# Kernel optimization log

Measured on AMD Instinct MI355X. Metric: run time of the kernel, lower is better.

## Reference

```python
import jax, jax.numpy as jnp
import numpy as np

# sparse_shape = grid_size[::-1] + [1,0,0] for grid_size=[1408,1600,40]
Z, Y, X = 41, 1600, 1408
N = 400000
CIN, COUT = 4, 16
EPS = 1e-3  # BatchNorm1d eps from partial(nn.BatchNorm1d, eps=0.001)


def setup_inputs() -> dict:
    # unique active voxel coordinates (submanifold conv assumes no duplicates)
    rng = np.random.default_rng(0)
    pool = Z * Y * X
    raw = rng.integers(0, pool, size=3 * N, dtype=np.int64)
    lin = np.unique(raw)[:N]
    assert lin.size == N
    z = lin // (Y * X)
    rem = lin % (Y * X)
    y = rem // X
    x = rem % X
    coords = np.stack([np.zeros(N, np.int64), z, y, x], axis=1).astype(np.int32)

    key = jax.random.key(0)
    k1, k2 = jax.random.split(key)
    voxel_features = jax.random.normal(k1, (N, CIN), dtype=jnp.float32)
    # SubMConv3d weight: one [CIN,COUT] matrix per kernel offset (27 = 3^3)
    weight = jax.random.normal(k2, (27, CIN, COUT), dtype=jnp.float32) * 0.1
    gamma = jnp.ones((COUT,), dtype=jnp.float32)
    beta = jnp.zeros((COUT,), dtype=jnp.float32)
    return {
        "voxel_features": voxel_features,
        "voxel_coords": jnp.asarray(coords),
        "weight": weight,
        "gamma": gamma,
        "beta": beta,
    }


_OFFSETS = jnp.asarray(
    np.stack(np.meshgrid([-1, 0, 1], [-1, 0, 1], [-1, 0, 1], indexing="ij"), -1
             ).reshape(27, 3),
    dtype=jnp.int32,
)


def _subm_conv(feats, coords, weight):
    """Submanifold sparse 3D conv: outputs only at active voxel sites.

    Rulebook built via sorted linear keys + searchsorted (gather-GEMM).
    """
    zyx = coords[:, 1:4].astype(jnp.int32)                 # [N,3]
    keys = (zyx[:, 0] * Y + zyx[:, 1]) * X + zyx[:, 2]     # [N] unique linear key
    order = jnp.argsort(keys)
    skeys = keys[order]

    nb = zyx[None, :, :] + _OFFSETS[:, None, :]            # [27,N,3]
    inb = ((nb >= 0).all(-1)
           & (nb[..., 0] < Z) & (nb[..., 1] < Y) & (nb[..., 2] < X))
    nkeys = (nb[..., 0] * Y + nb[..., 1]) * X + nb[..., 2]  # [27,N]
    pos = jnp.clip(jnp.searchsorted(skeys, nkeys), 0, N - 1)
    found = inb & (skeys[pos] == nkeys)                    # neighbor is active
    idx = order[pos]                                       # [27,N] row into feats

    gathered = jnp.where(found[..., None], feats[idx], 0.0)  # [27,N,CIN]
    return jnp.einsum("knc,kco->no", gathered, weight)       # [N,COUT]


def reference(voxel_features, voxel_coords, weight, gamma, beta):
    out = _subm_conv(voxel_features, voxel_coords, weight)
    # BatchNorm1d in training mode: normalize over the N (voxel) axis
    mu = out.mean(0)
    var = out.var(0)
    out = (out - mu) * jax.lax.rsqrt(var + EPS) * gamma + beta
    return jax.nn.relu(out)
```

## Files before the change

### kernel.cpp

```cpp
#include <hip/hip_runtime.h>
#include <stdint.h>

#define ZD 41
#define YD 1600
#define XD 1408
#define YXD (YD * XD)
#define NKEYS (ZD * YD * XD)
#define ENT_WORDS (NKEYS / 32)
#define BN_EPS 1e-3f

typedef unsigned long long u64;


__global__ void __launch_bounds__(256) build_index(
    const int4* __restrict__ coords, u64* __restrict__ entry, int n) {
  int i = blockIdx.x * blockDim.x + threadIdx.x;

  {
    int4 cl = coords[n - 1];
    int glast = (((cl.y * YD + cl.z) * XD + cl.w)) >> 5;
    int stride = gridDim.x * blockDim.x;
    for (int g = glast + 1 + i; g < ENT_WORDS; g += stride)
      entry[g] = (u64)(uint32_t)n;
  }

  if (i >= n) return;
  int4 c = coords[i];
  int key = (c.y * YD + c.z) * XD + c.w;
  int g = key >> 5;

  int pkey = __shfl_up(key, 1);
  if ((threadIdx.x & 63) == 0 && i > 0) {
    int4 cp = coords[i - 1];
    pkey = (cp.y * YD + cp.z) * XD + cp.w;
  }
  int pg = (i > 0) ? (pkey >> 5) : -1;

  if (g != pg) {
    for (int gg = pg + 1; gg < g; ++gg) entry[gg] = (u64)(uint32_t)i;
    uint32_t bits = 1u << (key & 31);
    int j = i + 1;
    while (j < n) {
      int4 cj = coords[j];
      int kj = (cj.y * YD + cj.z) * XD + cj.w;
      if ((kj >> 5) != g) break;
      bits |= 1u << (kj & 31);
      ++j;
    }
    entry[g] = ((u64)bits << 32) | (uint32_t)i;
  }
}

__global__ void __launch_bounds__(256) subm_conv(
    const float4* __restrict__ feats, const int4* __restrict__ coords,
    const float* __restrict__ weight, const u64* __restrict__ entry,
    float* __restrict__ out, float* __restrict__ partial, int n) {
  __shared__ float wl[27 * 64];
  __shared__ float swred[4][32];
  for (int t = threadIdx.x; t < 27 * 64; t += 256) wl[t] = weight[t];
  __syncthreads();

  int B = gridDim.x;
  int q = B >> 3, r = B & 7;
  int xcd = blockIdx.x & 7, off = blockIdx.x >> 3;
  int sb = (xcd < r ? xcd * (q + 1) : r * (q + 1) + (xcd - r) * q) + off;
  int i = sb * 256 + (int)threadIdx.x;

  float acc[16];
#pragma unroll
  for (int o = 0; o < 16; o++) acc[o] = 0.f;

  if (i < n) {
    int4 czyx = coords[i];
    int z = czyx.y, y = czyx.z, x = czyx.w;
    int key = (z * YD + y) * XD + x;

    {
      float4 fs = feats[i];
      const float* wp = &wl[13 * 64];
#pragma unroll
      for (int o = 0; o < 16; o++)
        acc[o] = fs.x * wp[o] + fs.y * wp[o + 16] + fs.z * wp[o + 32] +
                 fs.w * wp[o + 48];
    }

    unsigned mask27 = 0;
#pragma unroll
    for (int dzy = 0; dzy < 9; dzy++) {
      const int dz = dzy / 3 - 1, dy = dzy % 3 - 1;
      bool ok = ((unsigned)(z + dz) < (unsigned)ZD) &&
                ((unsigned)(y + dy) < (unsigned)YD);
      int base = key + dz * YXD + dy * XD - 1;
      int g0 = base >> 5;
      u64 e0 = 0, e1 = 0;
      if (ok) {
        e0 = entry[g0];
        e1 = entry[g0 + 1];
      }
      u64 W = (e0 >> 32) | (e1 & 0xFFFFFFFF00000000ull);
      unsigned m3 = (unsigned)(W >> (base & 31)) & 7u;
      mask27 |= m3 << (dzy * 3);
    }
    mask27 &= ~(1u << 13);
    if (x == 0) mask27 &= ~0x1249249u;
    if (x == XD - 1) mask27 &= ~0x4924924u;

    while (mask27) {
      int b = __ffs(mask27) - 1;
      mask27 &= mask27 - 1;
      int dzy = (b * 11) >> 5;
      int rem = b - dzy * 3;
      int dzq = (dzy * 11) >> 5;
      int dyr = dzy - dzq * 3;
      int s = key + (dzq - 1) * YXD + (dyr - 1) * XD + rem - 1;
      int gs = s >> 5;
      u64 e = entry[gs];
      int j = (int)(e & 0xFFFFFFFFull) +
              __popc((uint32_t)(e >> 32) & ((1u << (s & 31)) - 1u));
      float4 f = feats[j];
      const float* wp = &wl[b * 64];
#pragma unroll
      for (int o = 0; o < 16; o++)
        acc[o] += f.x * wp[o] + f.y * wp[o + 16] + f.z * wp[o + 32] +
                  f.w * wp[o + 48];
    }

    float4* o4 = (float4*)(out + (size_t)i * 16);
    o4[0] = make_float4(acc[0], acc[1], acc[2], acc[3]);
    o4[1] = make_float4(acc[4], acc[5], acc[6], acc[7]);
    o4[2] = make_float4(acc[8], acc[9], acc[10], acc[11]);
    o4[3] = make_float4(acc[12], acc[13], acc[14], acc[15]);
  }

  int lane = threadIdx.x & 63, wv = threadIdx.x >> 6;
#pragma unroll
  for (int o = 0; o < 16; o++) {
    float s = acc[o], qq = acc[o] * acc[o];
#pragma unroll
    for (int offx = 32; offx; offx >>= 1) {
      s += __shfl_xor(s, offx);
      qq += __shfl_xor(qq, offx);
    }
    if (lane == 0) {
      swred[wv][o] = s;
      swred[wv][16 + o] = qq;
    }
  }
  __syncthreads();
  if (threadIdx.x < 32) {
    float v = swred[0][threadIdx.x] + swred[1][threadIdx.x] +
              swred[2][threadIdx.x] + swred[3][threadIdx.x];
    partial[(size_t)blockIdx.x * 32 + threadIdx.x] = v;
  }
}

__global__ void __launch_bounds__(1024) bn_finalize(
    const float4* __restrict__ partial4, float* __restrict__ accum, int nb) {
  __shared__ float4 s4[1024];
  int t = threadIdx.x;
  int q = t & 7;
  int row0 = t >> 3;
  float4 v = make_float4(0.f, 0.f, 0.f, 0.f);
  for (int b = row0; b < nb; b += 128) {
    float4 p = partial4[(size_t)b * 8 + q];
    v.x += p.x;
    v.y += p.y;
    v.z += p.z;
    v.w += p.w;
  }
  s4[t] = v;
  __syncthreads();
  for (int half = 64; half >= 1; half >>= 1) {
    if (row0 < half) {
      float4 o = s4[t + half * 8];
      v.x += o.x;
      v.y += o.y;
      v.z += o.z;
      v.w += o.w;
      s4[t] = v;
    }
    __syncthreads();
  }
  if (t < 8) ((float4*)accum)[t] = s4[t];
}

__global__ void __launch_bounds__(256) bn_apply(
    float* __restrict__ out, const float* __restrict__ accum,
    const float* __restrict__ gamma, const float* __restrict__ beta, int n4,
    float invN) {
  __shared__ float sa[16], sb[16];
  int t = threadIdx.x;
  if (t < 16) {
    float mu = accum[t] * invN;
    float var = accum[16 + t] * invN - mu * mu;
    float inv = rsqrtf(var + BN_EPS);
    float a = gamma[t] * inv;
    sa[t] = a;
    sb[t] = beta[t] - mu * a;
  }
  __syncthreads();
  int i = blockIdx.x * 256 + t;
  if (i >= n4) return;
  float4* p = (float4*)out;
  float4 v = p[i];
  int c0 = (i & 3) * 4;
  v.x = fmaxf(v.x * sa[c0 + 0] + sb[c0 + 0], 0.f);
  v.y = fmaxf(v.y * sa[c0 + 1] + sb[c0 + 1], 0.f);
  v.z = fmaxf(v.z * sa[c0 + 2] + sb[c0 + 2], 0.f);
  v.w = fmaxf(v.w * sa[c0 + 3] + sb[c0 + 3], 0.f);
  p[i] = v;
}

extern "C" void kernel_launch(void* const* d_in, const int* in_sizes, int n_in,
                              void* d_out, int out_size, void* d_ws,
                              size_t ws_size, hipStream_t stream) {
  const float4* feats = (const float4*)d_in[0];
  const int4* coords = (const int4*)d_in[1];
  const float* weight = (const float*)d_in[2];
  const float* gamma = (const float*)d_in[3];
  const float* beta = (const float*)d_in[4];
  int n = in_sizes[0] / 4;

  float* accum = (float*)d_ws;
  u64* entry = (u64*)((char*)d_ws + 256);
  float* partial = (float*)((char*)d_ws + 256 + (size_t)ENT_WORDS * 8 + 16);

  int bb = (n + 255) / 256;
  hipLaunchKernelGGL(build_index, dim3(bb), dim3(256), 0, stream, coords,
                     entry, n);
  hipLaunchKernelGGL(subm_conv, dim3(bb), dim3(256), 0, stream, feats, coords,
                     weight, entry, (float*)d_out, partial, n);
  hipLaunchKernelGGL(bn_finalize, dim3(1), dim3(1024), 0, stream,
                     (const float4*)partial, accum, bb);
  int n4 = n * 4;
  hipLaunchKernelGGL(bn_apply, dim3((n4 + 255) / 256), dim3(256), 0, stream,
                     (float*)d_out, accum, gamma, beta, n4, 1.0f / n);
}
```

Measured before the change: 123.8 us.

## Fuse index build, conv, and batchnorm into one cooperative kernel with grid syncs

Replaces the four-kernel pipeline with one cooperative kernel. It builds the bitmap index, runs the sparse conv, reduces the BN statistics hierarchically and applies BN+ReLU, separated by grid.sync barriers. The conv outputs stay in registers until normalization, so the separate pass that reads and writes the output again is gone, along with the launch gaps. In exchange it needs the whole grid (about 1563 blocks) to be co-resident under launch_bounds(256,7), and it adds three grid-wide barriers. If residency cannot be met it falls back to the old path.

```diff
diff --git a/kernel.cpp b/kernel.cpp
--- a/kernel.cpp
+++ b/kernel.cpp
@@ -1,5 +1,8 @@
 #include <hip/hip_runtime.h>
+#include <hip/hip_cooperative_groups.h>
 #include <stdint.h>
+
+namespace cg = cooperative_groups;
 
 #define ZD 41
 #define YD 1600
@@ -12,59 +15,64 @@
 typedef unsigned long long u64;
 
 
-__global__ void __launch_bounds__(256) build_index(
-    const int4* __restrict__ coords, u64* __restrict__ entry, int n) {
-  int i = blockIdx.x * blockDim.x + threadIdx.x;
-
-  {
-    int4 cl = coords[n - 1];
-    int glast = (((cl.y * YD + cl.z) * XD + cl.w)) >> 5;
-    int stride = gridDim.x * blockDim.x;
-    for (int g = glast + 1 + i; g < ENT_WORDS; g += stride)
-      entry[g] = (u64)(uint32_t)n;
-  }
-
-  if (i >= n) return;
-  int4 c = coords[i];
-  int key = (c.y * YD + c.z) * XD + c.w;
-  int g = key >> 5;
-
-  int pkey = __shfl_up(key, 1);
-  if ((threadIdx.x & 63) == 0 && i > 0) {
-    int4 cp = coords[i - 1];
-    pkey = (cp.y * YD + cp.z) * XD + cp.w;
-  }
-  int pg = (i > 0) ? (pkey >> 5) : -1;
-
-  if (g != pg) {
-    for (int gg = pg + 1; gg < g; ++gg) entry[gg] = (u64)(uint32_t)i;
-    uint32_t bits = 1u << (key & 31);
-    int j = i + 1;
-    while (j < n) {
-      int4 cj = coords[j];
-      int kj = (cj.y * YD + cj.z) * XD + cj.w;
-      if ((kj >> 5) != g) break;
-      bits |= 1u << (kj & 31);
-      ++j;
-    }
-    entry[g] = ((u64)bits << 32) | (uint32_t)i;
-  }
-}
-
-__global__ void __launch_bounds__(256) subm_conv(
+__global__ void __launch_bounds__(256, 7) fused_all(
     const float4* __restrict__ feats, const int4* __restrict__ coords,
-    const float* __restrict__ weight, const u64* __restrict__ entry,
-    float* __restrict__ out, float* __restrict__ partial, int n) {
+    const float* __restrict__ weight, const float* __restrict__ gamma,
+    const float* __restrict__ beta, u64* __restrict__ entry,
+    float* __restrict__ partial, float* __restrict__ partial2,
+    float* __restrict__ out, int n, int nb, float invN) {
+  cg::grid_group grid = cg::this_grid();
+  const int tid = threadIdx.x;
+
   __shared__ float wl[27 * 64];
   __shared__ float swred[4][32];
-  for (int t = threadIdx.x; t < 27 * 64; t += 256) wl[t] = weight[t];
+  __shared__ float red2[8][32];
+  __shared__ float redv[32];
+  __shared__ float sa[16], sbv[16];
+
+  {
+    int ia = blockIdx.x * 256 + tid;
+    int4 cl = coords[n - 1];
+    int glast = ((cl.y * YD + cl.z) * XD + cl.w) >> 5;
+    int stride = gridDim.x * 256;
+    for (int g = glast + 1 + ia; g < ENT_WORDS; g += stride)
+      entry[g] = (u64)(uint32_t)n;
+    if (ia < n) {
+      int4 c = coords[ia];
+      int key = (c.y * YD + c.z) * XD + c.w;
+      int g = key >> 5;
+      int pkey = __shfl_up(key, 1);
+      if ((tid & 63) == 0 && ia > 0) {
+        int4 cp = coords[ia - 1];
+        pkey = (cp.y * YD + cp.z) * XD + cp.w;
+      }
+      int pg = (ia > 0) ? (pkey >> 5) : -1;
+      if (g != pg) {
+        for (int gg = pg + 1; gg < g; ++gg) entry[gg] = (u64)(uint32_t)ia;
+        uint32_t bits = 1u << (key & 31);
+        int j = ia + 1;
+        while (j < n) {
+          int4 cj = coords[j];
+          int kj = (cj.y * YD + cj.z) * XD + cj.w;
+          if ((kj >> 5) != g) break;
+          bits |= 1u << (kj & 31);
+          ++j;
+        }
+        entry[g] = ((u64)bits << 32) | (uint32_t)ia;
+      }
+    }
+  }
+  __threadfence();
+  grid.sync();
+
+  for (int t = tid; t < 27 * 64; t += 256) wl[t] = weight[t];
   __syncthreads();
 
   int B = gridDim.x;
   int q = B >> 3, r = B & 7;
   int xcd = blockIdx.x & 7, off = blockIdx.x >> 3;
-  int sb = (xcd < r ? xcd * (q + 1) : r * (q + 1) + (xcd - r) * q) + off;
-  int i = sb * 256 + (int)threadIdx.x;
+  int sbk = (xcd < r ? xcd * (q + 1) : r * (q + 1) + (xcd - r) * q) + off;
+  int i = sbk * 256 + tid;
 
   float acc[16];
 #pragma unroll
@@ -124,14 +132,207 @@
         acc[o] += f.x * wp[o] + f.y * wp[o + 16] + f.z * wp[o + 32] +
                   f.w * wp[o + 48];
     }
-
+  }
+
+  {
+    int lane = tid & 63, wv = tid >> 6;
+#pragma unroll
+    for (int o = 0; o < 16; o++) {
+      float s = acc[o], qq = acc[o] * acc[o];
+#pragma unroll
+      for (int offx = 32; offx; offx >>= 1) {
+        s += __shfl_xor(s, offx);
+        qq += __shfl_xor(qq, offx);
+      }
+      if (lane == 0) {
+        swred[wv][o] = s;
+        swred[wv][16 + o] = qq;
+      }
+    }
+    __syncthreads();
+    if (tid < 32) {
+      float v = swred[0][tid] + swred[1][tid] + swred[2][tid] + swred[3][tid];
+      partial[(size_t)blockIdx.x * 32 + tid] = v;
+    }
+  }
+  __threadfence();
+  grid.sync();
+
+  if (blockIdx.x < 64) {
+    int c = tid & 31, s = tid >> 5;
+    float v = 0.f;
+    for (int rr = blockIdx.x + 64 * s; rr < nb; rr += 512)
+      v += partial[(size_t)rr * 32 + c];
+    red2[s][c] = v;
+    __syncthreads();
+    if (tid < 32) {
+      float vv = 0.f;
+#pragma unroll
+      for (int k = 0; k < 8; k++) vv += red2[k][tid];
+      partial2[(size_t)blockIdx.x * 32 + tid] = vv;
+    }
+  }
+  __threadfence();
+  grid.sync();
+
+  {
+    int c = tid & 31, s = tid >> 5;
+    float v = 0.f;
+#pragma unroll
+    for (int k = 0; k < 8; k++) v += partial2[(size_t)(s + 8 * k) * 32 + c];
+    red2[s][c] = v;
+    __syncthreads();
+    if (tid < 32) {
+      float vv = 0.f;
+#pragma unroll
+      for (int k = 0; k < 8; k++) vv += red2[k][tid];
+      redv[tid] = vv;
+    }
+    __syncthreads();
+    if (tid < 16) {
+      float mu = redv[tid] * invN;
+      float var = redv[16 + tid] * invN - mu * mu;
+      float inv = rsqrtf(var + BN_EPS);
+      float a = gamma[tid] * inv;
+      sa[tid] = a;
+      sbv[tid] = beta[tid] - mu * a;
+    }
+    __syncthreads();
+    if (i < n) {
+      float4* o4 = (float4*)(out + (size_t)i * 16);
+      float4 t0, t1, t2, t3;
+      t0.x = fmaxf(acc[0] * sa[0] + sbv[0], 0.f);
+      t0.y = fmaxf(acc[1] * sa[1] + sbv[1], 0.f);
+      t0.z = fmaxf(acc[2] * sa[2] + sbv[2], 0.f);
+      t0.w = fmaxf(acc[3] * sa[3] + sbv[3], 0.f);
+      t1.x = fmaxf(acc[4] * sa[4] + sbv[4], 0.f);
+      t1.y = fmaxf(acc[5] * sa[5] + sbv[5], 0.f);
+      t1.z = fmaxf(acc[6] * sa[6] + sbv[6], 0.f);
+      t1.w = fmaxf(acc[7] * sa[7] + sbv[7], 0.f);
+      t2.x = fmaxf(acc[8] * sa[8] + sbv[8], 0.f);
+      t2.y = fmaxf(acc[9] * sa[9] + sbv[9], 0.f);
+      t2.z = fmaxf(acc[10] * sa[10] + sbv[10], 0.f);
+      t2.w = fmaxf(acc[11] * sa[11] + sbv[11], 0.f);
+      t3.x = fmaxf(acc[12] * sa[12] + sbv[12], 0.f);
+      t3.y = fmaxf(acc[13] * sa[13] + sbv[13], 0.f);
+      t3.z = fmaxf(acc[14] * sa[14] + sbv[14], 0.f);
+      t3.w = fmaxf(acc[15] * sa[15] + sbv[15], 0.f);
+      o4[0] = t0;
+      o4[1] = t1;
+      o4[2] = t2;
+      o4[3] = t3;
+    }
+  }
+}
+
+__global__ void __launch_bounds__(256) build_index(
+    const int4* __restrict__ coords, u64* __restrict__ entry, int n) {
+  int i = blockIdx.x * blockDim.x + threadIdx.x;
+  {
+    int4 cl = coords[n - 1];
+    int glast = (((cl.y * YD + cl.z) * XD + cl.w)) >> 5;
+    int stride = gridDim.x * blockDim.x;
+    for (int g = glast + 1 + i; g < ENT_WORDS; g += stride)
+      entry[g] = (u64)(uint32_t)n;
+  }
+  if (i >= n) return;
+  int4 c = coords[i];
+  int key = (c.y * YD + c.z) * XD + c.w;
+  int g = key >> 5;
+  int pkey = __shfl_up(key, 1);
+  if ((threadIdx.x & 63) == 0 && i > 0) {
+    int4 cp = coords[i - 1];
+    pkey = (cp.y * YD + cp.z) * XD + cp.w;
+  }
+  int pg = (i > 0) ? (pkey >> 5) : -1;
+  if (g != pg) {
+    for (int gg = pg + 1; gg < g; ++gg) entry[gg] = (u64)(uint32_t)i;
+    uint32_t bits = 1u << (key & 31);
+    int j = i + 1;
+    while (j < n) {
+      int4 cj = coords[j];
+      int kj = (cj.y * YD + cj.z) * XD + cj.w;
+      if ((kj >> 5) != g) break;
+      bits |= 1u << (kj & 31);
+      ++j;
+    }
+    entry[g] = ((u64)bits << 32) | (uint32_t)i;
+  }
+}
+
+__global__ void __launch_bounds__(256) subm_conv(
+    const float4* __restrict__ feats, const int4* __restrict__ coords,
+    const float* __restrict__ weight, const u64* __restrict__ entry,
+    float* __restrict__ out, float* __restrict__ partial, int n) {
+  __shared__ float wl[27 * 64];
+  __shared__ float swred[4][32];
+  for (int t = threadIdx.x; t < 27 * 64; t += 256) wl[t] = weight[t];
+  __syncthreads();
+  int B = gridDim.x;
+  int q = B >> 3, r = B & 7;
+  int xcd = blockIdx.x & 7, off = blockIdx.x >> 3;
+  int sb = (xcd < r ? xcd * (q + 1) : r * (q + 1) + (xcd - r) * q) + off;
+  int i = sb * 256 + (int)threadIdx.x;
+  float acc[16];
+#pragma unroll
+  for (int o = 0; o < 16; o++) acc[o] = 0.f;
+  if (i < n) {
+    int4 czyx = coords[i];
+    int z = czyx.y, y = czyx.z, x = czyx.w;
+    int key = (z * YD + y) * XD + x;
+    {
+      float4 fs = feats[i];
+      const float* wp = &wl[13 * 64];
+#pragma unroll
+      for (int o = 0; o < 16; o++)
+        acc[o] = fs.x * wp[o] + fs.y * wp[o + 16] + fs.z * wp[o + 32] +
+                 fs.w * wp[o + 48];
+    }
+    unsigned mask27 = 0;
+#pragma unroll
+    for (int dzy = 0; dzy < 9; dzy++) {
+      const int dz = dzy / 3 - 1, dy = dzy % 3 - 1;
+      bool ok = ((unsigned)(z + dz) < (unsigned)ZD) &&
+                ((unsigned)(y + dy) < (unsigned)YD);
+      int base = key + dz * YXD + dy * XD - 1;
+      int g0 = base >> 5;
+      u64 e0 = 0, e1 = 0;
+      if (ok) {
+        e0 = entry[g0];
+        e1 = entry[g0 + 1];
+      }
+      u64 W = (e0 >> 32) | (e1 & 0xFFFFFFFF00000000ull);
+      unsigned m3 = (unsigned)(W >> (base & 31)) & 7u;
+      mask27 |= m3 << (dzy * 3);
+    }
+    mask27 &= ~(1u << 13);
+    if (x == 0) mask27 &= ~0x1249249u;
+    if (x == XD - 1) mask27 &= ~0x4924924u;
+    while (mask27) {
+      int b = __ffs(mask27) - 1;
+      mask27 &= mask27 - 1;
+      int dzy = (b * 11) >> 5;
+      int rem = b - dzy * 3;
+      int dzq = (dzy * 11) >> 5;
+      int dyr = dzy - dzq * 3;
+      int s = key + (dzq - 1) * YXD + (dyr - 1) * XD + rem - 1;
+      int gs = s >> 5;
+      u64 e = entry[gs];
+      int j = (int)(e & 0xFFFFFFFFull) +
+              __popc((uint32_t)(e >> 32) & ((1u << (s & 31)) - 1u));
+      float4 f = feats[j];
+      const float* wp = &wl[b * 64];
+#pragma unroll
+      for (int o = 0; o < 16; o++)
+        acc[o] += f.x * wp[o] + f.y * wp[o + 16] + f.z * wp[o + 32] +
+                  f.w * wp[o + 48];
+    }
     float4* o4 = (float4*)(out + (size_t)i * 16);
     o4[0] = make_float4(acc[0], acc[1], acc[2], acc[3]);
     o4[1] = make_float4(acc[4], acc[5], acc[6], acc[7]);
     o4[2] = make_float4(acc[8], acc[9], acc[10], acc[11]);
     o4[3] = make_float4(acc[12], acc[13], acc[14], acc[15]);
   }
-
   int lane = threadIdx.x & 63, wv = threadIdx.x >> 6;
 #pragma unroll
   for (int o = 0; o < 16; o++) {
@@ -224,15 +425,31 @@
   float* accum = (float*)d_ws;
   u64* entry = (u64*)((char*)d_ws + 256);
   float* partial = (float*)((char*)d_ws + 256 + (size_t)ENT_WORDS * 8 + 16);
-
-  int bb = (n + 255) / 256;
-  hipLaunchKernelGGL(build_index, dim3(bb), dim3(256), 0, stream, coords,
-                     entry, n);
-  hipLaunchKernelGGL(subm_conv, dim3(bb), dim3(256), 0, stream, feats, coords,
-                     weight, entry, (float*)d_out, partial, n);
-  hipLaunchKernelGGL(bn_finalize, dim3(1), dim3(1024), 0, stream,
-                     (const float4*)partial, accum, bb);
-  int n4 = n * 4;
-  hipLaunchKernelGGL(bn_apply, dim3((n4 + 255) / 256), dim3(256), 0, stream,
-                     (float*)d_out, accum, gamma, beta, n4, 1.0f / n);
-}
+  int nb = (n + 255) / 256;
+  float* partial2 = partial + (size_t)nb * 32;
+  float* out = (float*)d_out;
+  float invN = 1.0f / n;
+
+  int maxB = 0, numCU = 0;
+  hipOccupancyMaxActiveBlocksPerMultiprocessor(&maxB, fused_all, 256, 0);
+  hipDeviceGetAttribute(&numCU, hipDeviceAttributeMultiprocessorCount, 0);
+
+  if ((long)maxB * numCU >= nb) {
+    void* args[] = {(void*)&feats, (void*)&coords,  (void*)&weight,
+                    (void*)&gamma, (void*)&beta,    (void*)&entry,
+                    (void*)&partial, (void*)&partial2, (void*)&out,
+                    (void*)&n,     (void*)&nb,      (void*)&invN};
+    hipLaunchCooperativeKernel((void*)fused_all, dim3(nb), dim3(256), args, 0,
+                               stream);
+  } else {
+    hipLaunchKernelGGL(build_index, dim3(nb), dim3(256), 0, stream, coords,
+                       entry, n);
+    hipLaunchKernelGGL(subm_conv, dim3(nb), dim3(256), 0, stream, feats,
+                       coords, weight, entry, out, partial, n);
+    hipLaunchKernelGGL(bn_finalize, dim3(1), dim3(1024), 0, stream,
+                       (const float4*)partial, accum, nb);
+    int n4 = n * 4;
+    hipLaunchKernelGGL(bn_apply, dim3((n4 + 255) / 256), dim3(256), 0, stream,
+                       out, accum, gamma, beta, n4, invN);
+  }
+}
```

New measurement: 124.3 us. About the same (+0.4%).
